# Optimization experiments

Hardware: AMD Instinct MI355X
Metric: run time of the kernel (lower is better)

## Reference

```python
import jax, jax.numpy as jnp
import numpy as np

B, H, W, C = 2, 256, 256, 192
HEADS, WIN, SHIFT = 6, 8, 4
HID = 4 * C
N = WIN * WIN            # tokens per window
HD = C // HEADS
SCALE = HD ** -0.5

# ---- static relative-position index (matches torch buffer construction) ----
_c = np.stack(np.meshgrid(np.arange(WIN), np.arange(WIN), indexing='ij')).reshape(2, -1)
_r = (_c[:, :, None] - _c[:, None, :]).transpose(1, 2, 0)
_r[..., 0] += WIN - 1
_r[..., 1] += WIN - 1
_r[..., 0] *= 2 * WIN - 1
RPI = _r.sum(-1)  # [N, N]

# ---- static shift attention mask (Swin-style region mask, shift_size>0) ----
def _build_shift_mask():
    m = np.zeros((H, W))
    cnt = 0
    sl = (slice(0, -WIN), slice(-WIN, -SHIFT), slice(-SHIFT, None))
    for hs in sl:
        for ws in sl:
            m[hs, ws] = cnt
            cnt += 1
    mw = m.reshape(H // WIN, WIN, W // WIN, WIN).transpose(0, 2, 1, 3).reshape(-1, N)
    am = mw[:, None, :] - mw[:, :, None]  # unsqueeze(1) - unsqueeze(2)
    return jnp.asarray(np.where(am != 0, -100.0, 0.0), jnp.float32)  # [nW, N, N]

ATTN_MASK = _build_shift_mask()

def _win_part(x):  # [B,H,W,c] -> [B*nW, N, c]
    b, c = x.shape[0], x.shape[-1]
    x = x.reshape(b, H // WIN, WIN, W // WIN, WIN, c).transpose(0, 1, 3, 2, 4, 5)
    return x.reshape(-1, N, c)

def _win_rev(w):  # [B*nW, N, c] -> [B,H,W,c]
    c = w.shape[-1]
    x = w.reshape(-1, H // WIN, W // WIN, WIN, WIN, c).transpose(0, 1, 3, 2, 4, 5)
    return x.reshape(-1, H, W, c)

def _ln(x, w, b):
    mu = x.mean(-1, keepdims=True)
    v = ((x - mu) ** 2).mean(-1, keepdims=True)
    return (x - mu) / jnp.sqrt(v + 1e-5) * w + b


def setup_inputs() -> dict:
    key = jax.random.key(0)
    ks = jax.random.split(key, 9)
    s = jnp.float32(0.02)
    f32 = jnp.float32
    return {
        'x': jax.random.normal(ks[0], (B, H * W, C), f32),
        'norm1_w': jnp.ones((C,), f32), 'norm1_b': jnp.zeros((C,), f32),
        'q_w': jax.random.normal(ks[1], (C, C), f32) * s, 'q_b': jnp.zeros((C,), f32),
        'kv_w': jax.random.normal(ks[2], (C, 2 * C), f32) * s, 'kv_b': jnp.zeros((2 * C,), f32),
        'rpb': jax.random.normal(ks[3], ((2 * WIN - 1) ** 2, HEADS), f32) * s,
        'proj_w': jax.random.normal(ks[4], (C, C), f32) * s, 'proj_b': jnp.zeros((C,), f32),
        'norm2_w': jnp.ones((C,), f32), 'norm2_b': jnp.zeros((C,), f32),
        'l1_w': jax.random.normal(ks[5], (C, HID), f32) * s, 'l1_b': jnp.zeros((HID,), f32),
        'dw_w': jax.random.normal(ks[6], (3, 3, 1, HID), f32) * s, 'dw_b': jnp.zeros((HID,), f32),
        'l2_w': jax.random.normal(ks[7], (HID, C), f32) * s, 'l2_b': jnp.zeros((C,), f32),
    }


def reference(x, norm1_w, norm1_b, q_w, q_b, kv_w, kv_b, rpb, proj_w, proj_b,
              norm2_w, norm2_b, l1_w, l1_b, dw_w, dw_b, l2_w, l2_b):
    shortcut = x
    xn = _ln(x, norm1_w, norm1_b)
    q = (xn @ q_w + q_b).reshape(B, H, W, C)
    kv = (xn @ kv_w + kv_b).reshape(B, H, W, 2 * C)
    # cyclic shift
    q = jnp.roll(q, (-SHIFT, -SHIFT), axis=(1, 2))
    kv = jnp.roll(kv, (-SHIFT, -SHIFT), axis=(1, 2))
    # window partition -> heads
    qw = _win_part(q).reshape(-1, N, HEADS, HD).transpose(0, 2, 1, 3)          # [B_,h,N,hd]
    kvw = _win_part(kv).reshape(-1, N, 2, HEADS, HD).transpose(2, 0, 3, 1, 4)
    kw, vw = kvw[0], kvw[1]
    attn = jnp.einsum('bhnd,bhmd->bhnm', qw * SCALE, kw)                       # [B_,h,N,N]
    bias = rpb[RPI.reshape(-1)].reshape(N, N, HEADS).transpose(2, 0, 1)        # [h,N,N]
    attn = attn + bias[None]
    nW = ATTN_MASK.shape[0]
    attn = attn.reshape(B, nW, HEADS, N, N) + ATTN_MASK[None, :, None]
    attn = jax.nn.softmax(attn.reshape(-1, HEADS, N, N), axis=-1)
    y = jnp.einsum('bhnm,bhmd->bnhd', attn, vw).reshape(-1, N, C)
    y = y @ proj_w + proj_b
    xa = _win_rev(y)
    xa = jnp.roll(xa, (SHIFT, SHIFT), axis=(1, 2)).reshape(B, H * W, C)
    x = shortcut + xa
    # LeFF: linear -> GELU -> 3x3 depthwise conv -> GELU -> linear
    xn = _ln(x, norm2_w, norm2_b)
    h = jax.nn.gelu(xn @ l1_w + l1_b, approximate=False).reshape(B, H, W, HID)
    h = jax.lax.conv_general_dilated(h, dw_w, (1, 1), 'SAME',
                                     dimension_numbers=('NHWC', 'HWIO', 'NHWC'),
                                     feature_group_count=HID) + dw_b
    h = jax.nn.gelu(h, approximate=False).reshape(B, H * W, HID)
    return x + (h @ l2_w + l2_b)
```

## Files before the change

kernel.cpp:

```cpp
#include <hip/hip_runtime.h>
#include <math.h>

typedef float f32x4 __attribute__((ext_vector_type(4)));
typedef short bf16x8 __attribute__((ext_vector_type(8)));
typedef short bf16x4 __attribute__((ext_vector_type(4)));

__device__ __forceinline__ short f2bf(float f) {
  unsigned u = __builtin_bit_cast(unsigned, f);
  u = (u + 0x7FFFu + ((u >> 16) & 1u)) >> 16;
  return (short)u;
}
__device__ __forceinline__ float bf2f(short s) {
  unsigned u = ((unsigned)(unsigned short)s) << 16;
  return __builtin_bit_cast(float, u);
}
__device__ __forceinline__ float gelu_exact(float x) {
  return 0.5f * x * (1.0f + erff(x * 0.70710678118654752f));
}
__device__ __forceinline__ void gld16(const short* g, short* l) {
  __builtin_amdgcn_global_load_lds(
      (const __attribute__((address_space(1))) void*)g,
      (__attribute__((address_space(3))) void*)l, 16, 0, 0);
}

__device__ __forceinline__ long perm_row(int b, int ho, int wo) {
  int hs = (ho + 252) & 255, ws = (wo + 252) & 255;
  int w = ((hs >> 3) << 5) | (ws >> 3);
  int t = ((hs & 7) << 3) | (ws & 7);
  return ((long)b << 16) | (w << 6) | t;
}
__device__ __forceinline__ long unperm_row(long m) {
  int b = (int)(m >> 16);
  int w = ((int)m >> 6) & 1023, t = (int)m & 63;
  int hs = ((w >> 5) << 3) | (t >> 3);
  int ws = ((w & 31) << 3) | (t & 7);
  int ho = (hs + 4) & 255, wo = (ws + 4) & 255;
  return ((long)b << 16) | (ho << 8) | wo;
}

__global__ __launch_bounds__(256) void ln1_kernel(const float* __restrict__ x,
                                                  const float* __restrict__ w,
                                                  const float* __restrict__ b,
                                                  short* __restrict__ out) {
  int lane = threadIdx.x & 63;
  long row = (long)blockIdx.x * 4 + (threadIdx.x >> 6);
  const float* xr = x + row * 192;
  float v0 = xr[lane], v1 = xr[lane + 64], v2 = xr[lane + 128];
  float s = v0 + v1 + v2, s2 = v0 * v0 + v1 * v1 + v2 * v2;
#pragma unroll
  for (int m = 1; m < 64; m <<= 1) {
    s += __shfl_xor(s, m);
    s2 += __shfl_xor(s2, m);
  }
  float mu = s * (1.0f / 192.0f);
  float rstd = rsqrtf(s2 * (1.0f / 192.0f) - mu * mu + 1e-5f);
  long drow = perm_row((int)(row >> 16), ((int)row >> 8) & 255, (int)row & 255);
  short* o = out + drow * 192;
  o[lane] = f2bf((v0 - mu) * rstd * w[lane] + b[lane]);
  o[lane + 64] = f2bf((v1 - mu) * rstd * w[lane + 64] + b[lane + 64]);
  o[lane + 128] = f2bf((v2 - mu) * rstd * w[lane + 128] + b[lane + 128]);
}

__global__ __launch_bounds__(256) void ln2_kernel(const short* __restrict__ x,
                                                  const float* __restrict__ w,
                                                  const float* __restrict__ b,
                                                  short* __restrict__ out) {
  int lane = threadIdx.x & 63;
  long row = (long)blockIdx.x * 4 + (threadIdx.x >> 6);
  const short* xr = x + row * 192;
  float v0 = bf2f(xr[lane]), v1 = bf2f(xr[lane + 64]), v2 = bf2f(xr[lane + 128]);
  float s = v0 + v1 + v2, s2 = v0 * v0 + v1 * v1 + v2 * v2;
#pragma unroll
  for (int m = 1; m < 64; m <<= 1) {
    s += __shfl_xor(s, m);
    s2 += __shfl_xor(s2, m);
  }
  float mu = s * (1.0f / 192.0f);
  float rstd = rsqrtf(s2 * (1.0f / 192.0f) - mu * mu + 1e-5f);
  short* o = out + row * 192;
  o[lane] = f2bf((v0 - mu) * rstd * w[lane] + b[lane]);
  o[lane + 64] = f2bf((v1 - mu) * rstd * w[lane + 64] + b[lane + 64]);
  o[lane + 128] = f2bf((v2 - mu) * rstd * w[lane + 128] + b[lane + 128]);
}

__global__ __launch_bounds__(256) void wprep_kernel(const float* __restrict__ w,
                                                    short* __restrict__ bt,
                                                    int K, int N) {
  long i = (long)blockIdx.x * 256 + threadIdx.x;
  if (i >= (long)K * N) return;
  int n = (int)(i / K), k = (int)(i % K);
  bt[i] = f2bf(w[(long)k * N + n]);
}

__global__ __launch_bounds__(256) void bias_prep(const float* __restrict__ rpb,
                                                 float* __restrict__ biasTab) {
  int i = blockIdx.x * 256 + threadIdx.x;
  int k = i & 63, q = (i >> 6) & 63, h = i >> 12;
  int dr = (q >> 3) - (k >> 3) + 7;
  int dc = (q & 7) - (k & 7) + 7;
  biasTab[i] = rpb[(dr * 15 + dc) * 6 + h] * 1.4426950408889634f;
}

__global__ __launch_bounds__(384) void fused_attn_kernel(
    const short* __restrict__ xn, const short* __restrict__ bt1,
    const short* __restrict__ bt2, const float* __restrict__ q_b,
    const float* __restrict__ kv_b, const float* __restrict__ proj_b,
    const float* __restrict__ residf, const float* __restrict__ biasTab,
    short* __restrict__ x2bf) {
  __shared__ short S_[57344];
  const int tid = threadIdx.x;
  const int lane = tid & 63, wid = tid >> 6;
  const int lr = lane & 15, lg = lane >> 4;
  const int bid = blockIdx.x;
  const int wglob = (bid & 7) * 256 + (bid >> 3);
  const int w = wglob & 1023;
  const int wr = w >> 5, wc = w & 31;
  const long wbase = (long)wglob * 64;
  const int RB = 12800 + wid * 7424;

#pragma unroll
  for (int p = 0; p < 4; ++p) {
    int g = p * 384 + tid;
    int r = g / 24, c = g % 24;
    *(float4*)(&S_[r * 200 + c * 8]) =
        *(const float4*)(xn + (wbase + r) * 192 + c * 8);
  }
  __syncthreads();

  {
    f32x4 acc[4][6] = {};
#pragma unroll
    for (int ks = 0; ks < 6; ++ks) {
      bf16x8 a[4], b[6];
#pragma unroll
      for (int mf = 0; mf < 4; ++mf)
        a[mf] = *(const bf16x8*)(&S_[(mf * 16 + lr) * 200 + ks * 32 + lg * 8]);
#pragma unroll
      for (int st = 0; st < 3; ++st)
#pragma unroll
        for (int nf = 0; nf < 2; ++nf)
          b[st * 2 + nf] = *(const bf16x8*)(
              bt1 + (long)(st * 192 + wid * 32 + nf * 16 + lr) * 192 +
              ks * 32 + lg * 8);
#pragma unroll
      for (int mf = 0; mf < 4; ++mf)
#pragma unroll
        for (int j = 0; j < 6; ++j)
          acc[mf][j] = __builtin_amdgcn_mfma_f32_16x16x32_bf16(
              a[mf], b[j], acc[mf][j], 0, 0, 0);
    }
#pragma unroll
    for (int mf = 0; mf < 4; ++mf) {
      int row0 = mf * 16 + lg * 4;
#pragma unroll
      for (int nf = 0; nf < 2; ++nf) {
        int c = nf * 16 + lr;
        float qb = q_b[wid * 32 + c];
        float kb = kv_b[wid * 32 + c];
        float vb = kv_b[192 + wid * 32 + c];
#pragma unroll
        for (int r = 0; r < 4; ++r) {
          S_[RB + (row0 + r) * 40 + c] = f2bf(acc[mf][nf][r] + qb);
          S_[RB + 2560 + (row0 + r) * 40 + c] = f2bf(acc[mf][2 + nf][r] + kb);
        }
        bf16x4 vv;
#pragma unroll
        for (int r = 0; r < 4; ++r) vv[r] = f2bf(acc[mf][4 + nf][r] + vb);
        *(bf16x4*)(&S_[RB + 5120 + c * 72 + row0]) = vv;
      }
    }
  }

  bf16x8 aq[4], bk[4];
#pragma unroll
  for (int i = 0; i < 4; ++i) {
    aq[i] = *(const bf16x8*)(&S_[RB + (i * 16 + lr) * 40 + lg * 8]);
    bk[i] = *(const bf16x8*)(&S_[RB + 2560 + (i * 16 + lr) * 40 + lg * 8]);
  }
  f32x4 s[4][4] = {};
#pragma unroll
  for (int mi = 0; mi < 4; ++mi)
#pragma unroll
    for (int ni = 0; ni < 4; ++ni)
      s[mi][ni] = __builtin_amdgcn_mfma_f32_16x16x32_bf16(aq[mi], bk[ni],
                                                          s[mi][ni], 0, 0, 0);

  const float SCL2 = 0.17677669529663687f * 1.4426950408889634f;
  const float MASKC = -144.26950408889634f;
  const bool edge = (wr == 31) || (wc == 31);
  int ridk[4] = {0, 0, 0, 0};
  if (edge) {
#pragma unroll
    for (int ni = 0; ni < 4; ++ni) {
      int k = ni * 16 + lr;
      int kh = wr * 8 + (k >> 3), kw = wc * 8 + (k & 7);
      ridk[ni] = 3 * ((kh < 248) ? 0 : ((kh < 252) ? 1 : 2)) +
                 ((kw < 248) ? 0 : ((kw < 252) ? 1 : 2));
    }
  }
  float rinv[4][4];
#pragma unroll
  for (int mi = 0; mi < 4; ++mi) {
#pragma unroll
    for (int r = 0; r < 4; ++r) {
      int q = mi * 16 + lg * 4 + r;
      const float* bp = biasTab + (wid << 12) + (q << 6);
      int ridq = 0;
      if (edge) {
        int qh = wr * 8 + (q >> 3), qw = wc * 8 + (q & 7);
        ridq = 3 * ((qh < 248) ? 0 : ((qh < 252) ? 1 : 2)) +
               ((qw < 248) ? 0 : ((qw < 252) ? 1 : 2));
      }
      float lv[4];
      float mx = -1e30f;
#pragma unroll
      for (int ni = 0; ni < 4; ++ni) {
        float lvv = s[mi][ni][r] * SCL2 + bp[ni * 16 + lr];
        if (edge && ridq != ridk[ni]) lvv += MASKC;
        lv[ni] = lvv;
        mx = fmaxf(mx, lvv);
      }
#pragma unroll
      for (int m = 1; m < 16; m <<= 1) mx = fmaxf(mx, __shfl_xor(mx, m));
      float sum = 0.0f;
#pragma unroll
      for (int ni = 0; ni < 4; ++ni) {
        float p = exp2f(lv[ni] - mx);
        lv[ni] = p;
        sum += p;
      }
#pragma unroll
      for (int m = 1; m < 16; m <<= 1) sum += __shfl_xor(sum, m);
      rinv[mi][r] = 1.0f / sum;
#pragma unroll
      for (int ni = 0; ni < 4; ++ni)
        S_[RB + q * 72 + ni * 16 + lr] = f2bf(lv[ni]);
    }
  }

  f32x4 o[4][2] = {};
#pragma unroll
  for (int ks = 0; ks < 2; ++ks) {
    bf16x8 ap[4], bv[2];
#pragma unroll
    for (int mi = 0; mi < 4; ++mi)
      ap[mi] = *(const bf16x8*)(&S_[RB + (mi * 16 + lr) * 72 + ks * 32 +
                                    lg * 8]);
#pragma unroll
    for (int ni = 0; ni < 2; ++ni)
      bv[ni] = *(const bf16x8*)(&S_[RB + 5120 + (ni * 16 + lr) * 72 +
                                    ks * 32 + lg * 8]);
#pragma unroll
    for (int mi = 0; mi < 4; ++mi)
#pragma unroll
      for (int ni = 0; ni < 2; ++ni)
        o[mi][ni] = __builtin_amdgcn_mfma_f32_16x16x32_bf16(ap[mi], bv[ni],
                                                            o[mi][ni], 0, 0, 0);
  }
#pragma unroll
  for (int mi = 0; mi < 4; ++mi)
#pragma unroll
    for (int r = 0; r < 4; ++r) {
      int q = mi * 16 + lg * 4 + r;
      float ri = rinv[mi][r];
#pragma unroll
      for (int ni = 0; ni < 2; ++ni)
        S_[RB + q * 40 + ni * 16 + lr] = f2bf(o[mi][ni][r] * ri);
    }
  __syncthreads();

  {
    f32x4 acc[4][2] = {};
#pragma unroll
    for (int ks = 0; ks < 6; ++ks) {
      bf16x8 a[4], bq[2];
#pragma unroll
      for (int mf = 0; mf < 4; ++mf)
        a[mf] = *(const bf16x8*)(&S_[12800 + ks * 7424 +
                                     (mf * 16 + lr) * 40 + lg * 8]);
#pragma unroll
      for (int nf = 0; nf < 2; ++nf)
        bq[nf] = *(const bf16x8*)(bt2 +
                                  (long)(wid * 32 + nf * 16 + lr) * 192 +
                                  ks * 32 + lg * 8);
#pragma unroll
      for (int mf = 0; mf < 4; ++mf)
#pragma unroll
        for (int nf = 0; nf < 2; ++nf)
          acc[mf][nf] = __builtin_amdgcn_mfma_f32_16x16x32_bf16(
              a[mf], bq[nf], acc[mf][nf], 0, 0, 0);
    }
#pragma unroll
    for (int mf = 0; mf < 4; ++mf)
#pragma unroll
      for (int nf = 0; nf < 2; ++nf) {
        int n = wid * 32 + nf * 16 + lr;
#pragma unroll
        for (int r = 0; r < 4; ++r) {
          long m = wbase + mf * 16 + lg * 4 + r;
          long oidx = unperm_row(m) * 192 + n;
          x2bf[oidx] = f2bf(acc[mf][nf][r] + proj_b[n] + residf[oidx]);
        }
      }
  }
}

template <int NTOT, int EPI>
__global__ __launch_bounds__(256) void gemm1_kernel(
    const short* __restrict__ A, const short* __restrict__ Bt,
    const float* __restrict__ B0, short* __restrict__ outp,
    int nblk, int mgx, int iters, int mtiles) {
  __shared__ short As[128 * 192];
  const int tid = threadIdx.x;
  const int lane = tid & 63, wid = tid >> 6;
  const int lr = lane & 15, lg = lane >> 4;
  const int xcd = blockIdx.x & 7;
  const int i = blockIdx.x >> 3;
  const int n0 = (i % nblk) * 64;
  const int mg = xcd * mgx + i / nblk;

  bf16x8 bf[6][4];
#pragma unroll
  for (int ks = 0; ks < 6; ++ks)
#pragma unroll
    for (int ni = 0; ni < 4; ++ni)
      bf[ks][ni] = *(const bf16x8*)(Bt + (long)(n0 + ni * 16 + lr) * 192 +
                                    ks * 32 + lg * 8);

  int src_s[12];
#pragma unroll
  for (int s = 0; s < 12; ++s) {
    int lo = (wid * 12 + s) * 1024 + lane * 16;
    int r = lo / 384, c = lo % 384;
    src_s[s] = r * 192 + ((c ^ ((r & 7) << 4)) >> 1);
  }
  const int xorv = (lr & 7) << 4;

#pragma unroll 1
  for (int it = 0; it < iters; ++it) {
    int mt = mg * iters + it;
    if (mt >= mtiles) continue;
    long m0 = (long)mt * 128;
    const short* Ab = A + m0 * 192;
    __syncthreads();
#pragma unroll
    for (int s = 0; s < 12; ++s)
      gld16(Ab + src_s[s], As + (wid * 12 + s) * 512);
    __syncthreads();
    f32x4 acc[2][4] = {};
#pragma unroll
    for (int ks = 0; ks < 6; ++ks) {
      const char* asb = (const char*)As;
      const int col = (ks * 64 + lg * 16) ^ xorv;
      bf16x8 a0 = *(const bf16x8*)(asb + (wid * 32 + lr) * 384 + col);
      bf16x8 a1 = *(const bf16x8*)(asb + (wid * 32 + 16 + lr) * 384 + col);
#pragma unroll
      for (int ni = 0; ni < 4; ++ni) {
        acc[0][ni] = __builtin_amdgcn_mfma_f32_16x16x32_bf16(a0, bf[ks][ni],
                                                             acc[0][ni], 0, 0, 0);
        acc[1][ni] = __builtin_amdgcn_mfma_f32_16x16x32_bf16(a1, bf[ks][ni],
                                                             acc[1][ni], 0, 0, 0);
      }
    }
#pragma unroll
    for (int mi = 0; mi < 2; ++mi) {
#pragma unroll
      for (int ni = 0; ni < 4; ++ni) {
        int n = n0 + ni * 16 + lr;
        long rowb = m0 + wid * 32 + mi * 16 + lg * 4;
#pragma unroll
        for (int r = 0; r < 4; ++r) {
          long m = rowb + r;
          outp[m * NTOT + n] = f2bf(gelu_exact(acc[mi][ni][r] + B0[n]));
        }
      }
    }
  }
}

__global__ __launch_bounds__(256) void gemm2_kernel(
    const short* __restrict__ A, const short* __restrict__ Bt,
    const float* __restrict__ bias, const short* __restrict__ residb,
    float* __restrict__ outp) {
  __shared__ short As[128][72];
  __shared__ short Bs[192][72];
  const int tid = threadIdx.x;
  const int lane = tid & 63, wid = tid >> 6;
  const int lr = lane & 15, lg = lane >> 4;
  const int wm = wid >> 1, wn = wid & 1;
  const long m0 = (long)blockIdx.x * 128;

  f32x4 acc[4][6] = {};
#pragma unroll 1
  for (int kc = 0; kc < 12; ++kc) {
    __syncthreads();
#pragma unroll
    for (int p = 0; p < 4; ++p) {
      int g = p * 256 + tid;
      int r = g >> 3, c = g & 7;
      *(float4*)(&As[r][c * 8]) =
          *(const float4*)(A + (m0 + r) * 768 + kc * 64 + c * 8);
    }
#pragma unroll
    for (int p = 0; p < 6; ++p) {
      int g = p * 256 + tid;
      int n = g >> 3, c = g & 7;
      *(float4*)(&Bs[n][c * 8]) =
          *(const float4*)(Bt + (long)n * 768 + kc * 64 + c * 8);
    }
    __syncthreads();
#pragma unroll
    for (int ks = 0; ks < 2; ++ks) {
      bf16x8 a[4], b[6];
#pragma unroll
      for (int mf = 0; mf < 4; ++mf)
        a[mf] = *(const bf16x8*)(&As[wm * 64 + mf * 16 + lr][ks * 32 + lg * 8]);
#pragma unroll
      for (int nf = 0; nf < 6; ++nf)
        b[nf] = *(const bf16x8*)(&Bs[wn * 96 + nf * 16 + lr][ks * 32 + lg * 8]);
#pragma unroll
      for (int mf = 0; mf < 4; ++mf)
#pragma unroll
        for (int nf = 0; nf < 6; ++nf)
          acc[mf][nf] = __builtin_amdgcn_mfma_f32_16x16x32_bf16(
              a[mf], b[nf], acc[mf][nf], 0, 0, 0);
    }
  }
#pragma unroll
  for (int mf = 0; mf < 4; ++mf)
#pragma unroll
    for (int nf = 0; nf < 6; ++nf) {
      int n = wn * 96 + nf * 16 + lr;
      long rowb = m0 + wm * 64 + mf * 16 + lg * 4;
#pragma unroll
      for (int r = 0; r < 4; ++r) {
        long idx = (rowb + r) * 192 + n;
        outp[idx] = acc[mf][nf][r] + bias[n] + bf2f(residb[idx]);
      }
    }
}

__global__ __launch_bounds__(256) void dwconv_kernel(const short* __restrict__ hbc,
                                                     const float* __restrict__ dww,
                                                     const float* __restrict__ dwb,
                                                     short* __restrict__ h2c,
                                                     int yh) {
  int t = blockIdx.x * 256 + threadIdx.x;
  int cg = t % 96;
  int px = t / 96;
  int strip = blockIdx.y;

  float wv[9][8];
#pragma unroll
  for (int tap = 0; tap < 9; ++tap) {
    float4 a = *(const float4*)(dww + tap * 768 + cg * 8);
    float4 b = *(const float4*)(dww + tap * 768 + cg * 8 + 4);
    wv[tap][0] = a.x; wv[tap][1] = a.y; wv[tap][2] = a.z; wv[tap][3] = a.w;
    wv[tap][4] = b.x; wv[tap][5] = b.y; wv[tap][6] = b.z; wv[tap][7] = b.w;
  }
  float bias[8];
  {
    float4 a = *(const float4*)(dwb + cg * 8);
    float4 b = *(const float4*)(dwb + cg * 8 + 4);
    bias[0] = a.x; bias[1] = a.y; bias[2] = a.z; bias[3] = a.w;
    bias[4] = b.x; bias[5] = b.y; bias[6] = b.z; bias[7] = b.w;
  }

#pragma unroll 2
  for (int pp = 0; pp < 16; ++pp) {
    int py = strip * 16 + pp;
    int ybase = yh * 128 + py;
    float acc[8];
#pragma unroll
    for (int j = 0; j < 8; ++j) acc[j] = bias[j];
#pragma unroll
    for (int dy = 0; dy < 3; ++dy) {
      int yy = ybase + dy - 1;
      if (yy < 0 || yy > 255) continue;
      int slot = py + dy;
#pragma unroll
      for (int dx = 0; dx < 3; ++dx) {
        int xx = px + dx - 1;
        if (xx < 0 || xx > 255) continue;
        bf16x8 hv = *(const bf16x8*)(hbc + ((long)slot * 256 + xx) * 768 + cg * 8);
#pragma unroll
        for (int j = 0; j < 8; ++j) acc[j] += bf2f(hv[j]) * wv[dy * 3 + dx][j];
      }
    }
    bf16x8 ov;
#pragma unroll
    for (int j = 0; j < 8; ++j) ov[j] = f2bf(gelu_exact(acc[j]));
    *(bf16x8*)(h2c + ((long)py * 256 + px) * 768 + cg * 8) = ov;
  }
}

extern "C" void kernel_launch(void* const* d_in, const int* in_sizes, int n_in,
                              void* d_out, int out_size, void* d_ws, size_t ws_size,
                              hipStream_t stream) {
  const float* x = (const float*)d_in[0];
  const float* n1w = (const float*)d_in[1];
  const float* n1b = (const float*)d_in[2];
  const float* q_w = (const float*)d_in[3];
  const float* q_b = (const float*)d_in[4];
  const float* kv_w = (const float*)d_in[5];
  const float* kv_b = (const float*)d_in[6];
  const float* rpb = (const float*)d_in[7];
  const float* proj_w = (const float*)d_in[8];
  const float* proj_b = (const float*)d_in[9];
  const float* n2w = (const float*)d_in[10];
  const float* n2b = (const float*)d_in[11];
  const float* l1_w = (const float*)d_in[12];
  const float* l1_b = (const float*)d_in[13];
  const float* dw_w = (const float*)d_in[14];
  const float* dw_b = (const float*)d_in[15];
  const float* l2_w = (const float*)d_in[16];
  const float* l2_b = (const float*)d_in[17];
  float* out = (float*)d_out;

  char* ws = (char*)d_ws;
  short* xn = (short*)ws;
  short* hbc = (short*)(ws + 50331648);
  short* h2c = (short*)(ws + 101449728);
  short* x2bf = (short*)(ws + 201326592);
  short* bt1 = (short*)(ws + 251658240);
  short* bt2 = bt1 + 110592;
  short* bt3 = bt2 + 36864;
  short* bt4 = bt3 + 147456;
  float* biasTab = (float*)(ws + 252542976);
  short* xn2 = xn;

  wprep_kernel<<<144, 256, 0, stream>>>(q_w, bt1, 192, 192);
  wprep_kernel<<<288, 256, 0, stream>>>(kv_w, bt1 + 36864, 192, 384);
  wprep_kernel<<<144, 256, 0, stream>>>(proj_w, bt2, 192, 192);
  wprep_kernel<<<576, 256, 0, stream>>>(l1_w, bt3, 192, 768);
  wprep_kernel<<<576, 256, 0, stream>>>(l2_w, bt4, 768, 192);
  bias_prep<<<96, 256, 0, stream>>>(rpb, biasTab);

  ln1_kernel<<<32768, 256, 0, stream>>>(x, n1w, n1b, xn);
  fused_attn_kernel<<<2048, 384, 0, stream>>>(xn, bt1, bt2, q_b, kv_b, proj_b,
                                              x, biasTab, x2bf);
  ln2_kernel<<<32768, 256, 0, stream>>>(x2bf, n2w, n2b, xn2);

  for (int c = 0; c < 4; ++c) {
    int b = c >> 1, yh = c & 1;
    int ystart = yh ? 127 : 0;
    int s0 = yh ? 0 : 1;
    long tok0 = (long)b * 65536 + (long)ystart * 256;
    long ooff = ((long)b * 65536 + (long)yh * 32768) * 192;
    gemm1_kernel<768, 2><<<864, 256, 0, stream>>>(
        xn2 + tok0 * 192, bt3, l1_b, hbc + (long)s0 * 196608, 12, 9, 4, 258);
    dwconv_kernel<<<dim3(96, 8), 256, 0, stream>>>(hbc, dw_w, dw_b, h2c, yh);
    gemm2_kernel<<<256, 256, 0, stream>>>(h2c, bt4, l2_b, x2bf + ooff,
                                          out + ooff);
  }
}
```

Measured before the change: 783.4 us.

## Fuse depthwise conv and GELU into the second LeFF GEMM's A-tile load

Drops the separate dwconv kernel and its h2c intermediate. The second GEMM now computes the 3x3 depthwise conv plus GELU for each 64-channel K-chunk directly into shared memory, with the conv weights staged in LDS. The chunked processing also goes from four half-image pieces to one whole image per batch, with gemm1 writing the full hidden tensor. The N dimension is split across two blocks, so each block recomputes the conv for its rows, doubling the conv work. Larger shared memory use may lower occupancy.

```diff
diff --git a/kernel.cpp b/kernel.cpp
--- a/kernel.cpp
+++ b/kernel.cpp
@@ -378,50 +378,100 @@
   }
 }
 
-__global__ __launch_bounds__(256) void gemm2_kernel(
-    const short* __restrict__ A, const short* __restrict__ Bt,
-    const float* __restrict__ bias, const short* __restrict__ residb,
-    float* __restrict__ outp) {
+__global__ __launch_bounds__(256) void gemm2f_kernel(
+    const short* __restrict__ hbc, const short* __restrict__ bt4,
+    const float* __restrict__ dww, const float* __restrict__ dwb,
+    const float* __restrict__ l2b, const short* __restrict__ x2bf_b,
+    float* __restrict__ out_b) {
+  __shared__ float wbuf[9 * 768];
+  __shared__ float bbuf[768];
   __shared__ short As[128][72];
-  __shared__ short Bs[192][72];
+  __shared__ short Bs[96][72];
   const int tid = threadIdx.x;
   const int lane = tid & 63, wid = tid >> 6;
   const int lr = lane & 15, lg = lane >> 4;
+  const int wg = (blockIdx.x & 7) * 128 + (blockIdx.x >> 3);
+  const int hr = wg >> 1;
+  const int nb = wg & 1;
+  const int py = hr >> 1;
+  const int pxb = (hr & 1) * 128;
+  const long rowbase = (long)py * 256 + pxb;
+  const int grp = tid & 7, ps = tid >> 3;
   const int wm = wid >> 1, wn = wid & 1;
-  const long m0 = (long)blockIdx.x * 128;
-
-  f32x4 acc[4][6] = {};
+
+#pragma unroll
+  for (int p = 0; p < 7; ++p) {
+    int g = p * 256 + tid;
+    if (g < 1728) *(float4*)(&wbuf[g * 4]) = *(const float4*)(dww + g * 4);
+  }
+  if (tid < 192) *(float4*)(&bbuf[tid * 4]) = *(const float4*)(dwb + tid * 4);
+
+  f32x4 acc[4][3] = {};
 #pragma unroll 1
   for (int kc = 0; kc < 12; ++kc) {
     __syncthreads();
 #pragma unroll
-    for (int p = 0; p < 4; ++p) {
-      int g = p * 256 + tid;
-      int r = g >> 3, c = g & 7;
-      *(float4*)(&As[r][c * 8]) =
-          *(const float4*)(A + (m0 + r) * 768 + kc * 64 + c * 8);
-    }
-#pragma unroll
-    for (int p = 0; p < 6; ++p) {
+    for (int p = 0; p < 3; ++p) {
       int g = p * 256 + tid;
       int n = g >> 3, c = g & 7;
       *(float4*)(&Bs[n][c * 8]) =
-          *(const float4*)(Bt + (long)n * 768 + kc * 64 + c * 8);
+          *(const float4*)(bt4 + (long)(nb * 96 + n) * 768 + kc * 64 + c * 8);
+    }
+    float wv[9][8];
+#pragma unroll
+    for (int tap = 0; tap < 9; ++tap) {
+      float4 a = *(float4*)(&wbuf[tap * 768 + kc * 64 + grp * 8]);
+      float4 b = *(float4*)(&wbuf[tap * 768 + kc * 64 + grp * 8 + 4]);
+      wv[tap][0] = a.x; wv[tap][1] = a.y; wv[tap][2] = a.z; wv[tap][3] = a.w;
+      wv[tap][4] = b.x; wv[tap][5] = b.y; wv[tap][6] = b.z; wv[tap][7] = b.w;
+    }
+    float bias8[8];
+    {
+      float4 a = *(float4*)(&bbuf[kc * 64 + grp * 8]);
+      float4 b = *(float4*)(&bbuf[kc * 64 + grp * 8 + 4]);
+      bias8[0] = a.x; bias8[1] = a.y; bias8[2] = a.z; bias8[3] = a.w;
+      bias8[4] = b.x; bias8[5] = b.y; bias8[6] = b.z; bias8[7] = b.w;
+    }
+#pragma unroll
+    for (int i = 0; i < 4; ++i) {
+      int p = ps + 32 * i;
+      int px = pxb + p;
+      float a8[8];
+#pragma unroll
+      for (int j = 0; j < 8; ++j) a8[j] = bias8[j];
+#pragma unroll
+      for (int dy = 0; dy < 3; ++dy) {
+        int yy = py + dy - 1;
+        if (yy < 0 || yy > 255) continue;
+#pragma unroll
+        for (int dx = 0; dx < 3; ++dx) {
+          int xx = px + dx - 1;
+          if (xx < 0 || xx > 255) continue;
+          bf16x8 hv = *(const bf16x8*)(hbc + ((long)yy * 256 + xx) * 768 +
+                                       kc * 64 + grp * 8);
+#pragma unroll
+          for (int j = 0; j < 8; ++j) a8[j] += bf2f(hv[j]) * wv[dy * 3 + dx][j];
+        }
+      }
+      bf16x8 ov;
+#pragma unroll
+      for (int j = 0; j < 8; ++j) ov[j] = f2bf(gelu_exact(a8[j]));
+      *(bf16x8*)(&As[p][grp * 8]) = ov;
     }
     __syncthreads();
 #pragma unroll
     for (int ks = 0; ks < 2; ++ks) {
-      bf16x8 a[4], b[6];
+      bf16x8 a[4], b[3];
 #pragma unroll
       for (int mf = 0; mf < 4; ++mf)
         a[mf] = *(const bf16x8*)(&As[wm * 64 + mf * 16 + lr][ks * 32 + lg * 8]);
 #pragma unroll
-      for (int nf = 0; nf < 6; ++nf)
-        b[nf] = *(const bf16x8*)(&Bs[wn * 96 + nf * 16 + lr][ks * 32 + lg * 8]);
+      for (int nf = 0; nf < 3; ++nf)
+        b[nf] = *(const bf16x8*)(&Bs[wn * 48 + nf * 16 + lr][ks * 32 + lg * 8]);
 #pragma unroll
       for (int mf = 0; mf < 4; ++mf)
 #pragma unroll
-        for (int nf = 0; nf < 6; ++nf)
+        for (int nf = 0; nf < 3; ++nf)
           acc[mf][nf] = __builtin_amdgcn_mfma_f32_16x16x32_bf16(
               a[mf], b[nf], acc[mf][nf], 0, 0, 0);
     }
@@ -429,69 +479,15 @@
 #pragma unroll
   for (int mf = 0; mf < 4; ++mf)
 #pragma unroll
-    for (int nf = 0; nf < 6; ++nf) {
-      int n = wn * 96 + nf * 16 + lr;
-      long rowb = m0 + wm * 64 + mf * 16 + lg * 4;
+    for (int nf = 0; nf < 3; ++nf) {
+      int n = nb * 96 + wn * 48 + nf * 16 + lr;
+      long rowb = rowbase + wm * 64 + mf * 16 + lg * 4;
 #pragma unroll
       for (int r = 0; r < 4; ++r) {
         long idx = (rowb + r) * 192 + n;
-        outp[idx] = acc[mf][nf][r] + bias[n] + bf2f(residb[idx]);
-      }
-    }
-}
-
-__global__ __launch_bounds__(256) void dwconv_kernel(const short* __restrict__ hbc,
-                                                     const float* __restrict__ dww,
-                                                     const float* __restrict__ dwb,
-                                                     short* __restrict__ h2c,
-                                                     int yh) {
-  int t = blockIdx.x * 256 + threadIdx.x;
-  int cg = t % 96;
-  int px = t / 96;
-  int strip = blockIdx.y;
-
-  float wv[9][8];
-#pragma unroll
-  for (int tap = 0; tap < 9; ++tap) {
-    float4 a = *(const float4*)(dww + tap * 768 + cg * 8);
-    float4 b = *(const float4*)(dww + tap * 768 + cg * 8 + 4);
-    wv[tap][0] = a.x; wv[tap][1] = a.y; wv[tap][2] = a.z; wv[tap][3] = a.w;
-    wv[tap][4] = b.x; wv[tap][5] = b.y; wv[tap][6] = b.z; wv[tap][7] = b.w;
-  }
-  float bias[8];
-  {
-    float4 a = *(const float4*)(dwb + cg * 8);
-    float4 b = *(const float4*)(dwb + cg * 8 + 4);
-    bias[0] = a.x; bias[1] = a.y; bias[2] = a.z; bias[3] = a.w;
-    bias[4] = b.x; bias[5] = b.y; bias[6] = b.z; bias[7] = b.w;
-  }
-
-#pragma unroll 2
-  for (int pp = 0; pp < 16; ++pp) {
-    int py = strip * 16 + pp;
-    int ybase = yh * 128 + py;
-    float acc[8];
-#pragma unroll
-    for (int j = 0; j < 8; ++j) acc[j] = bias[j];
-#pragma unroll
-    for (int dy = 0; dy < 3; ++dy) {
-      int yy = ybase + dy - 1;
-      if (yy < 0 || yy > 255) continue;
-      int slot = py + dy;
-#pragma unroll
-      for (int dx = 0; dx < 3; ++dx) {
-        int xx = px + dx - 1;
-        if (xx < 0 || xx > 255) continue;
-        bf16x8 hv = *(const bf16x8*)(hbc + ((long)slot * 256 + xx) * 768 + cg * 8);
-#pragma unroll
-        for (int j = 0; j < 8; ++j) acc[j] += bf2f(hv[j]) * wv[dy * 3 + dx][j];
-      }
-    }
-    bf16x8 ov;
-#pragma unroll
-    for (int j = 0; j < 8; ++j) ov[j] = f2bf(gelu_exact(acc[j]));
-    *(bf16x8*)(h2c + ((long)py * 256 + px) * 768 + cg * 8) = ov;
-  }
+        out_b[idx] = acc[mf][nf][r] + l2b[n] + bf2f(x2bf_b[idx]);
+      }
+    }
 }
 
 extern "C" void kernel_launch(void* const* d_in, const int* in_sizes, int n_in,
@@ -520,7 +516,6 @@
   char* ws = (char*)d_ws;
   short* xn = (short*)ws;
   short* hbc = (short*)(ws + 50331648);
-  short* h2c = (short*)(ws + 101449728);
   short* x2bf = (short*)(ws + 201326592);
   short* bt1 = (short*)(ws + 251658240);
   short* bt2 = bt1 + 110592;
@@ -541,16 +536,11 @@
                                               x, biasTab, x2bf);
   ln2_kernel<<<32768, 256, 0, stream>>>(x2bf, n2w, n2b, xn2);
 
-  for (int c = 0; c < 4; ++c) {
-    int b = c >> 1, yh = c & 1;
-    int ystart = yh ? 127 : 0;
-    int s0 = yh ? 0 : 1;
-    long tok0 = (long)b * 65536 + (long)ystart * 256;
-    long ooff = ((long)b * 65536 + (long)yh * 32768) * 192;
-    gemm1_kernel<768, 2><<<864, 256, 0, stream>>>(
-        xn2 + tok0 * 192, bt3, l1_b, hbc + (long)s0 * 196608, 12, 9, 4, 258);
-    dwconv_kernel<<<dim3(96, 8), 256, 0, stream>>>(hbc, dw_w, dw_b, h2c, yh);
-    gemm2_kernel<<<256, 256, 0, stream>>>(h2c, bt4, l2_b, x2bf + ooff,
-                                          out + ooff);
-  }
-}
+  for (int b = 0; b < 2; ++b) {
+    long toff = (long)b * 65536 * 192;
+    gemm1_kernel<768, 2><<<1536, 256, 0, stream>>>(
+        xn2 + toff, bt3, l1_b, hbc, 12, 16, 4, 512);
+    gemm2f_kernel<<<1024, 256, 0, stream>>>(hbc, bt4, dw_w, dw_b, l2_b,
+                                            x2bf + toff, out + toff);
+  }
+}
```

Result: slower. 1.013 ms (+29.3%).
